# Performance work log

Hardware: AMD Instinct MI355X
Metric: run time of the kernel (lower is better)

Reference implementation:

```python
import jax, jax.numpy as jnp
import numpy as np

N_NODES = 50000
N_EDGES = 800000
D_FEAT = 128
K_HOPS = 2


def setup_inputs() -> dict:
    key = jax.random.key(0)
    k1, k2, k3 = jax.random.split(key, 3)
    features = jax.random.normal(k1, (N_NODES, D_FEAT), dtype=jnp.float32)
    src = jax.random.randint(k2, (N_EDGES,), 0, N_NODES, dtype=jnp.int64)
    dst = jax.random.randint(k3, (N_EDGES,), 0, N_NODES, dtype=jnp.int64)
    return {"features": features, "src": src, "dst": dst}


def reference(features, src, dst):
    """SGCLayer: k=2 hops, degree-normalized copy_u/sum aggregation, mean layer aggr."""
    n = features.shape[0]
    # in_degrees: number of incoming edges per node, clamped to >= 1
    deg = jax.ops.segment_sum(jnp.ones(dst.shape, dtype=features.dtype), dst,
                              num_segments=n)
    norm = jnp.power(jnp.clip(deg, 1.0), -0.5)[:, None]  # [N, 1]
    h = features
    results = [features]
    for _ in range(K_HOPS):
        h = h * norm                   # pre-scale by D^-1/2
        m = h[src]                     # copy_u: gather source features [E, F]
        h = jax.ops.segment_sum(m, dst, num_segments=n)  # sum into dst [N, F]
        h = h * norm                   # post-scale by D^-1/2
        results.append(h)
    # layer_aggr == 'mean': average over the k+1 propagated representations
    H = jnp.stack(results, axis=1)     # [N, k+1, F]
    return jnp.mean(H, axis=1)
```

## Files before the change

### kernel.cpp

```cpp
#include <hip/hip_runtime.h>

#define N_NODES 50000
#define N_EDGES 800000
#define D_FEAT  128
#define CNT_STRIDE 16
#define ELL_CAP 64

typedef unsigned int uint;
typedef unsigned short ushort_t;

union f32u { float f; uint u; };

__device__ __forceinline__ ushort_t f2bf(float f) {
    f32u x; x.f = f;
    uint u = x.u;
    return (ushort_t)((u + 0x7FFFu + ((u >> 16) & 1u)) >> 16);
}

__global__ void zero_cnt(int4* __restrict__ cnt4) {
    int i = blockIdx.x * 256 + threadIdx.x;
    if (i < N_NODES * CNT_STRIDE / 4) cnt4[i] = make_int4(0, 0, 0, 0);
}

__global__ void prep(const float4* __restrict__ feat4, const int* __restrict__ dst,
                     const int* __restrict__ src, int* __restrict__ cnt,
                     int* __restrict__ ell, ushort4* __restrict__ featb4) {
    int gid = blockIdx.x * 256 + threadIdx.x;
    bool edge = (gid < N_EDGES);
    int d = 0, p = 0;
    if (edge) {
        d = dst[gid];
        p = atomicAdd(&cnt[d * CNT_STRIDE], 1);
    }
    if (gid < N_NODES * (D_FEAT / 4)) {
        float4 v = feat4[gid];
        ushort4 o;
        o.x = f2bf(v.x); o.y = f2bf(v.y); o.z = f2bf(v.z); o.w = f2bf(v.w);
        featb4[gid] = o;
    }
    if (edge && p < ELL_CAP) ell[d * ELL_CAP + p] = src[gid];
}

__global__ void norm_scale(const int* __restrict__ cnt, float* __restrict__ norm,
                           uint4* __restrict__ featb4) {
    int j = blockIdx.x * 256 + threadIdx.x;
    if (j < N_NODES * (D_FEAT / 8)) {
        int n = j >> 4;
        int deg = cnt[n * CNT_STRIDE];
        float nn = rsqrtf((float)(deg < 1 ? 1 : deg));
        uint4 v = featb4[j];
        f32u l0, h0, l1, h1, l2, h2, l3, h3;
        l0.u = v.x << 16; h0.u = v.x & 0xFFFF0000u;
        l1.u = v.y << 16; h1.u = v.y & 0xFFFF0000u;
        l2.u = v.z << 16; h2.u = v.z & 0xFFFF0000u;
        l3.u = v.w << 16; h3.u = v.w & 0xFFFF0000u;
        uint4 o;
        o.x = (uint)f2bf(l0.f * nn) | ((uint)f2bf(h0.f * nn) << 16);
        o.y = (uint)f2bf(l1.f * nn) | ((uint)f2bf(h1.f * nn) << 16);
        o.z = (uint)f2bf(l2.f * nn) | ((uint)f2bf(h2.f * nn) << 16);
        o.w = (uint)f2bf(l3.f * nn) | ((uint)f2bf(h3.f * nn) << 16);
        featb4[j] = o;
        if (j < N_NODES) {
            int dj = cnt[j * CNT_STRIDE];
            norm[j] = rsqrtf((float)(dj < 1 ? 1 : dj));
        }
    }
}

template<int FINAL>
__global__ void hop_gather(const int* __restrict__ ell, const int* __restrict__ cnt,
                           const ushort_t* __restrict__ hb, const float* __restrict__ norm,
                           const float* __restrict__ feat, const ushort_t* __restrict__ s1,
                           void* __restrict__ outp) {
    int node = blockIdx.x * 4 + (threadIdx.x >> 6);
    int lane = threadIdx.x & 63;
    int q    = lane >> 4;
    int l16  = lane & 15;
    const uint4* hbv = (const uint4*)hb;
    int b    = node * ELL_CAP;
    int ecnt = cnt[node * CNT_STRIDE];
    if (ecnt > ELL_CAP) ecnt = ELL_CAP;
    float a0 = 0, a1 = 0, a2 = 0, a3 = 0, a4 = 0, a5 = 0, a6 = 0, a7 = 0;

#define ACC2(P, E_, O_) { f32u lo_, hi_; lo_.u = (P) << 16; hi_.u = (P) & 0xFFFF0000u; \
                          E_ += lo_.f; O_ += hi_.f; }
#define ACCV(V) { ACC2(V.x, a0, a1); ACC2(V.y, a2, a3); ACC2(V.z, a4, a5); ACC2(V.w, a6, a7); }

    int i = 0;
    for (; i + 16 <= ecnt; i += 16) {
        int s0 = ell[b + i      + q];
        int s1i = ell[b + i + 4  + q];
        int s2 = ell[b + i + 8  + q];
        int s3 = ell[b + i + 12 + q];
        uint4 v0 = hbv[s0 * 16 + l16];
        uint4 v1 = hbv[s1i * 16 + l16];
        uint4 v2 = hbv[s2 * 16 + l16];
        uint4 v3 = hbv[s3 * 16 + l16];
        ACCV(v0); ACCV(v1); ACCV(v2); ACCV(v3);
    }
    if (i + 8 <= ecnt) {
        int s0 = ell[b + i     + q];
        int s1i = ell[b + i + 4 + q];
        uint4 v0 = hbv[s0 * 16 + l16];
        uint4 v1 = hbv[s1i * 16 + l16];
        ACCV(v0); ACCV(v1);
        i += 8;
    }
    if (i + 4 <= ecnt) {
        int s_ = ell[b + i + q];
        uint4 v_ = hbv[s_ * 16 + l16];
        ACCV(v_);
        i += 4;
    }
    int rem = ecnt - i;
    if (q < rem) {
        int s_ = ell[b + i + q];
        uint4 v_ = hbv[s_ * 16 + l16];
        ACCV(v_);
    }
#undef ACCV
#undef ACC2

    a0 += __shfl_xor(a0, 16, 64); a1 += __shfl_xor(a1, 16, 64);
    a2 += __shfl_xor(a2, 16, 64); a3 += __shfl_xor(a3, 16, 64);
    a4 += __shfl_xor(a4, 16, 64); a5 += __shfl_xor(a5, 16, 64);
    a6 += __shfl_xor(a6, 16, 64); a7 += __shfl_xor(a7, 16, 64);
    a0 += __shfl_xor(a0, 32, 64); a1 += __shfl_xor(a1, 32, 64);
    a2 += __shfl_xor(a2, 32, 64); a3 += __shfl_xor(a3, 32, 64);
    a4 += __shfl_xor(a4, 32, 64); a5 += __shfl_xor(a5, 32, 64);
    a6 += __shfl_xor(a6, 32, 64); a7 += __shfl_xor(a7, 32, 64);

    if (q == 0) {
        float nn = norm[node];
        if (!FINAL) {
            float n2 = nn * nn;
            uint4 o;
            o.x = (uint)f2bf(a0 * n2) | ((uint)f2bf(a1 * n2) << 16);
            o.y = (uint)f2bf(a2 * n2) | ((uint)f2bf(a3 * n2) << 16);
            o.z = (uint)f2bf(a4 * n2) | ((uint)f2bf(a5 * n2) << 16);
            o.w = (uint)f2bf(a6 * n2) | ((uint)f2bf(a7 * n2) << 16);
            ((uint4*)outp)[node * 16 + l16] = o;
        } else {
            float inv = 1.0f / nn;
            uint4 p = ((const uint4*)s1)[node * 16 + l16];
            f32u t0, t1, t2, t3, t4, t5, t6, t7;
            t0.u = p.x << 16; t1.u = p.x & 0xFFFF0000u;
            t2.u = p.y << 16; t3.u = p.y & 0xFFFF0000u;
            t4.u = p.z << 16; t5.u = p.z & 0xFFFF0000u;
            t6.u = p.w << 16; t7.u = p.w & 0xFFFF0000u;
            const float4* f4 = (const float4*)feat;
            float4 fA = f4[node * 32 + 2 * l16];
            float4 fB = f4[node * 32 + 2 * l16 + 1];
            const float third = 1.0f / 3.0f;
            float4 rA, rB;
            rA.x = (fA.x + t0.f * inv + nn * a0) * third;
            rA.y = (fA.y + t1.f * inv + nn * a1) * third;
            rA.z = (fA.z + t2.f * inv + nn * a2) * third;
            rA.w = (fA.w + t3.f * inv + nn * a3) * third;
            rB.x = (fB.x + t4.f * inv + nn * a4) * third;
            rB.y = (fB.y + t5.f * inv + nn * a5) * third;
            rB.z = (fB.z + t6.f * inv + nn * a6) * third;
            rB.w = (fB.w + t7.f * inv + nn * a7) * third;
            ((float4*)outp)[node * 32 + 2 * l16]     = rA;
            ((float4*)outp)[node * 32 + 2 * l16 + 1] = rB;
        }
    }
}

extern "C" void kernel_launch(void* const* d_in, const int* in_sizes, int n_in,
                              void* d_out, int out_size, void* d_ws, size_t ws_size,
                              hipStream_t stream) {
    const float* feat = (const float*)d_in[0];
    const int*   src  = (const int*)d_in[1];
    const int*   dst  = (const int*)d_in[2];
    float* out = (float*)d_out;

    char* ws = (char*)d_ws;
    int*      cnt   = (int*)     (ws + 0x0000000);
    float*    norm  = (float*)   (ws + 0x0310000);
    int*      ell   = (int*)     (ws + 0x0350000);
    ushort_t* featb = (ushort_t*)(ws + 0x1000000);
    ushort_t* s1b   = (ushort_t*)(ws + 0x1D00000);

    zero_cnt<<<(N_NODES * CNT_STRIDE / 4 + 255) / 256, 256, 0, stream>>>((int4*)cnt);
    prep<<<(N_NODES * (D_FEAT / 4) + 255) / 256, 256, 0, stream>>>(
        (const float4*)feat, dst, src, cnt, ell, (ushort4*)featb);
    norm_scale<<<(N_NODES * (D_FEAT / 8) + 255) / 256, 256, 0, stream>>>(
        cnt, norm, (uint4*)featb);

    hop_gather<0><<<N_NODES / 4, 256, 0, stream>>>(ell, cnt, featb, norm,
                                                   nullptr, nullptr, s1b);
    hop_gather<1><<<N_NODES / 4, 256, 0, stream>>>(ell, cnt, s1b, norm,
                                                   feat, s1b, out);
}
```

Before: 122.2 us.

## Build ELL via two-level bucket staging with LDS histogram instead of global atomics

Replaces per-edge global atomicAdd on a padded count array with a two-pass bucketing scheme. In the first pass, wave ballots group edges by coarse destination bucket and write packed (local dst, src) pairs into aliased staging buffers. In the second pass, one 1024-thread block per bucket ranks edges with shared-memory atomics and writes the ELL table and compact counts. This removes 800K contended global atomics and the zeroing of a large padded count array. In exchange the second pass runs on only 13 blocks, which badly underuses the GPU and may serialize. Staging slots are capped at 5120, so buckets with more edges than that silently drop them. The 16-bit packing of src assumes node ids below 65536.

```diff
diff --git a/kernel.cpp b/kernel.cpp
--- a/kernel.cpp
+++ b/kernel.cpp
@@ -3,8 +3,10 @@
 #define N_NODES 50000
 #define N_EDGES 800000
 #define D_FEAT  128
-#define CNT_STRIDE 16
 #define ELL_CAP 64
+#define NBKT 13
+#define NALIAS 16
+#define STAGE_CAP 5120
 
 typedef unsigned int uint;
 typedef unsigned short ushort_t;
@@ -17,28 +19,80 @@
     return (ushort_t)((u + 0x7FFFu + ((u >> 16) & 1u)) >> 16);
 }
 
-__global__ void zero_cnt(int4* __restrict__ cnt4) {
-    int i = blockIdx.x * 256 + threadIdx.x;
-    if (i < N_NODES * CNT_STRIDE / 4) cnt4[i] = make_int4(0, 0, 0, 0);
+__global__ void zero_bcnt(int* __restrict__ bcnt) {
+    int i = threadIdx.x;
+    if (i < NBKT * NALIAS) bcnt[i] = 0;
 }
 
 __global__ void prep(const float4* __restrict__ feat4, const int* __restrict__ dst,
-                     const int* __restrict__ src, int* __restrict__ cnt,
-                     int* __restrict__ ell, ushort4* __restrict__ featb4) {
+                     const int* __restrict__ src, int* __restrict__ bcnt,
+                     uint* __restrict__ stage, ushort4* __restrict__ featb4) {
     int gid = blockIdx.x * 256 + threadIdx.x;
-    bool edge = (gid < N_EDGES);
-    int d = 0, p = 0;
-    if (edge) {
-        d = dst[gid];
-        p = atomicAdd(&cnt[d * CNT_STRIDE], 1);
-    }
+    int lane = threadIdx.x & 63;
+    bool valid = (gid < N_EDGES);
+    int d = 0;
+    if (valid) d = dst[gid];
+    int mybkt = d >> 12;
+    unsigned long long my_mask = 0;
+#pragma unroll
+    for (int b = 0; b < NBKT; b++) {
+        unsigned long long m = __ballot(valid && (mybkt == b));
+        if (mybkt == b) my_mask = m;
+    }
+    int leader = __ffsll(my_mask) - 1;
+    if (leader < 0) leader = 0;
+    int grpcnt = __popcll(my_mask);
+    int alias = blockIdx.x & (NALIAS - 1);
+    int base_reg = 0;
+    if (valid && lane == leader)
+        base_reg = atomicAdd(&bcnt[mybkt * NALIAS + alias], grpcnt);
+
     if (gid < N_NODES * (D_FEAT / 4)) {
         float4 v = feat4[gid];
         ushort4 o;
         o.x = f2bf(v.x); o.y = f2bf(v.y); o.z = f2bf(v.z); o.w = f2bf(v.w);
         featb4[gid] = o;
     }
-    if (edge && p < ELL_CAP) ell[d * ELL_CAP + p] = src[gid];
+
+    int base = __shfl(base_reg, leader, 64);
+    int rank = __popcll(my_mask & ((1ull << lane) - 1));
+    if (valid) {
+        int slot = base + rank;
+        if (slot < STAGE_CAP) {
+            int s = src[gid];
+            stage[(mybkt * NALIAS + alias) * STAGE_CAP + slot] =
+                ((uint)(d & 4095) << 16) | (uint)s;
+        }
+    }
+}
+
+__global__ __launch_bounds__(1024) void bucket_rank(const int* __restrict__ bcnt,
+                                                    const uint* __restrict__ stage,
+                                                    int* __restrict__ ell,
+                                                    int* __restrict__ cnt) {
+    __shared__ int hist[4096];
+    int b = blockIdx.x;
+    for (int i = threadIdx.x; i < 4096; i += 1024) hist[i] = 0;
+    __syncthreads();
+    for (int a = 0; a < NALIAS; a++) {
+        int n = bcnt[b * NALIAS + a];
+        if (n > STAGE_CAP) n = STAGE_CAP;
+        const uint* sp = stage + (b * NALIAS + a) * STAGE_CAP;
+        for (int i = threadIdx.x; i < n; i += 1024) {
+            uint v = sp[i];
+            int ldst = v >> 16;
+            int s = (int)(v & 0xFFFFu);
+            int p = atomicAdd(&hist[ldst], 1);
+            if (p < ELL_CAP)
+                ell[(((b << 12) + ldst) << 6) + p] = s;
+        }
+    }
+    __syncthreads();
+    int base_node = b << 12;
+    for (int i = threadIdx.x; i < 4096; i += 1024) {
+        int n = base_node + i;
+        if (n < N_NODES) cnt[n] = hist[i];
+    }
 }
 
 __global__ void norm_scale(const int* __restrict__ cnt, float* __restrict__ norm,
@@ -46,7 +100,7 @@
     int j = blockIdx.x * 256 + threadIdx.x;
     if (j < N_NODES * (D_FEAT / 8)) {
         int n = j >> 4;
-        int deg = cnt[n * CNT_STRIDE];
+        int deg = cnt[n];
         float nn = rsqrtf((float)(deg < 1 ? 1 : deg));
         uint4 v = featb4[j];
         f32u l0, h0, l1, h1, l2, h2, l3, h3;
@@ -61,7 +115,7 @@
         o.w = (uint)f2bf(l3.f * nn) | ((uint)f2bf(h3.f * nn) << 16);
         featb4[j] = o;
         if (j < N_NODES) {
-            int dj = cnt[j * CNT_STRIDE];
+            int dj = cnt[j];
             norm[j] = rsqrtf((float)(dj < 1 ? 1 : dj));
         }
     }
@@ -78,7 +132,7 @@
     int l16  = lane & 15;
     const uint4* hbv = (const uint4*)hb;
     int b    = node * ELL_CAP;
-    int ecnt = cnt[node * CNT_STRIDE];
+    int ecnt = cnt[node];
     if (ecnt > ELL_CAP) ecnt = ELL_CAP;
     float a0 = 0, a1 = 0, a2 = 0, a3 = 0, a4 = 0, a5 = 0, a6 = 0, a7 = 0;
 
@@ -176,15 +230,18 @@
     float* out = (float*)d_out;
 
     char* ws = (char*)d_ws;
-    int*      cnt   = (int*)     (ws + 0x0000000);
-    float*    norm  = (float*)   (ws + 0x0310000);
-    int*      ell   = (int*)     (ws + 0x0350000);
-    ushort_t* featb = (ushort_t*)(ws + 0x1000000);
-    ushort_t* s1b   = (ushort_t*)(ws + 0x1D00000);
-
-    zero_cnt<<<(N_NODES * CNT_STRIDE / 4 + 255) / 256, 256, 0, stream>>>((int4*)cnt);
+    int*      bcnt  = (int*)     (ws + 0x0000000);
+    int*      cnt   = (int*)     (ws + 0x0010000);
+    float*    norm  = (float*)   (ws + 0x0050000);
+    uint*     stage = (uint*)    (ws + 0x0090000);
+    int*      ell   = (int*)     (ws + 0x0500000);
+    ushort_t* featb = (ushort_t*)(ws + 0x1200000);
+    ushort_t* s1b   = (ushort_t*)(ws + 0x1F00000);
+
+    zero_bcnt<<<1, 256, 0, stream>>>(bcnt);
     prep<<<(N_NODES * (D_FEAT / 4) + 255) / 256, 256, 0, stream>>>(
-        (const float4*)feat, dst, src, cnt, ell, (ushort4*)featb);
+        (const float4*)feat, dst, src, bcnt, stage, (ushort4*)featb);
+    bucket_rank<<<NBKT, 1024, 0, stream>>>(bcnt, stage, ell, cnt);
     norm_scale<<<(N_NODES * (D_FEAT / 8) + 255) / 256, 256, 0, stream>>>(
         cnt, norm, (uint4*)featb);
 
```

Result: slower. 380.3 us (+211.2%).

## Build ELL adjacency via per-block LDS histograms over destination ranges

Applied to the files above, without the earlier changes.

Replaces the global-atomic ELL build, which needed a zeroing kernel and a strided count array, with 64 blocks that each scan all edges and use shared-memory atomics for their own 784-node destination range. Degree counts and norms are written directly, and the bf16 conversion is fused with the norm pre-scale into a single kernel. This removes two launches and the contention from global atomics. In exchange every block re-reads the full src/dst arrays (64x redundant reads), and only 64 blocks run, so parallelism across the GPU is low.

```diff
diff --git a/kernel.cpp b/kernel.cpp
--- a/kernel.cpp
+++ b/kernel.cpp
@@ -3,8 +3,9 @@
 #define N_NODES 50000
 #define N_EDGES 800000
 #define D_FEAT  128
-#define CNT_STRIDE 16
 #define ELL_CAP 64
+#define NB 64
+#define RANGE 784
 
 typedef unsigned int uint;
 typedef unsigned short ushort_t;
@@ -17,53 +18,48 @@
     return (ushort_t)((u + 0x7FFFu + ((u >> 16) & 1u)) >> 16);
 }
 
-__global__ void zero_cnt(int4* __restrict__ cnt4) {
-    int i = blockIdx.x * 256 + threadIdx.x;
-    if (i < N_NODES * CNT_STRIDE / 4) cnt4[i] = make_int4(0, 0, 0, 0);
+__global__ __launch_bounds__(256) void ell_build(const int4* __restrict__ src4,
+                                                 const int4* __restrict__ dst4,
+                                                 int* __restrict__ ell,
+                                                 int* __restrict__ cnt,
+                                                 float* __restrict__ norm) {
+    __shared__ int hist[RANGE];
+    int lo = blockIdx.x * RANGE;
+    for (int i = threadIdx.x; i < RANGE; i += 256) hist[i] = 0;
+    __syncthreads();
+    for (int i = threadIdx.x; i < N_EDGES / 4; i += 256) {
+        int4 d4 = dst4[i];
+        int4 s4 = src4[i];
+#define DO(c) { int d_ = d4.c; unsigned r_ = (unsigned)(d_ - lo);              \
+                if (r_ < RANGE) {                                              \
+                    int p_ = atomicAdd(&hist[r_], 1);                          \
+                    if (p_ < ELL_CAP) ell[d_ * ELL_CAP + p_] = s4.c;           \
+                } }
+        DO(x) DO(y) DO(z) DO(w)
+#undef DO
+    }
+    __syncthreads();
+    for (int i = threadIdx.x; i < RANGE; i += 256) {
+        int n = lo + i;
+        if (n < N_NODES) {
+            int c = hist[i];
+            cnt[n] = c;
+            norm[n] = rsqrtf((float)(c < 1 ? 1 : c));
+        }
+    }
 }
 
-__global__ void prep(const float4* __restrict__ feat4, const int* __restrict__ dst,
-                     const int* __restrict__ src, int* __restrict__ cnt,
-                     int* __restrict__ ell, ushort4* __restrict__ featb4) {
+__global__ void convert_scale(const float4* __restrict__ feat4,
+                              const float* __restrict__ norm,
+                              ushort4* __restrict__ featb4) {
     int gid = blockIdx.x * 256 + threadIdx.x;
-    bool edge = (gid < N_EDGES);
-    int d = 0, p = 0;
-    if (edge) {
-        d = dst[gid];
-        p = atomicAdd(&cnt[d * CNT_STRIDE], 1);
-    }
     if (gid < N_NODES * (D_FEAT / 4)) {
+        float nn = norm[gid >> 5];
         float4 v = feat4[gid];
         ushort4 o;
-        o.x = f2bf(v.x); o.y = f2bf(v.y); o.z = f2bf(v.z); o.w = f2bf(v.w);
+        o.x = f2bf(v.x * nn); o.y = f2bf(v.y * nn);
+        o.z = f2bf(v.z * nn); o.w = f2bf(v.w * nn);
         featb4[gid] = o;
-    }
-    if (edge && p < ELL_CAP) ell[d * ELL_CAP + p] = src[gid];
-}
-
-__global__ void norm_scale(const int* __restrict__ cnt, float* __restrict__ norm,
-                           uint4* __restrict__ featb4) {
-    int j = blockIdx.x * 256 + threadIdx.x;
-    if (j < N_NODES * (D_FEAT / 8)) {
-        int n = j >> 4;
-        int deg = cnt[n * CNT_STRIDE];
-        float nn = rsqrtf((float)(deg < 1 ? 1 : deg));
-        uint4 v = featb4[j];
-        f32u l0, h0, l1, h1, l2, h2, l3, h3;
-        l0.u = v.x << 16; h0.u = v.x & 0xFFFF0000u;
-        l1.u = v.y << 16; h1.u = v.y & 0xFFFF0000u;
-        l2.u = v.z << 16; h2.u = v.z & 0xFFFF0000u;
-        l3.u = v.w << 16; h3.u = v.w & 0xFFFF0000u;
-        uint4 o;
-        o.x = (uint)f2bf(l0.f * nn) | ((uint)f2bf(h0.f * nn) << 16);
-        o.y = (uint)f2bf(l1.f * nn) | ((uint)f2bf(h1.f * nn) << 16);
-        o.z = (uint)f2bf(l2.f * nn) | ((uint)f2bf(h2.f * nn) << 16);
-        o.w = (uint)f2bf(l3.f * nn) | ((uint)f2bf(h3.f * nn) << 16);
-        featb4[j] = o;
-        if (j < N_NODES) {
-            int dj = cnt[j * CNT_STRIDE];
-            norm[j] = rsqrtf((float)(dj < 1 ? 1 : dj));
-        }
     }
 }
 
@@ -78,7 +74,7 @@
     int l16  = lane & 15;
     const uint4* hbv = (const uint4*)hb;
     int b    = node * ELL_CAP;
-    int ecnt = cnt[node * CNT_STRIDE];
+    int ecnt = cnt[node];
     if (ecnt > ELL_CAP) ecnt = ELL_CAP;
     float a0 = 0, a1 = 0, a2 = 0, a3 = 0, a4 = 0, a5 = 0, a6 = 0, a7 = 0;
 
@@ -177,16 +173,15 @@
 
     char* ws = (char*)d_ws;
     int*      cnt   = (int*)     (ws + 0x0000000);
-    float*    norm  = (float*)   (ws + 0x0310000);
-    int*      ell   = (int*)     (ws + 0x0350000);
-    ushort_t* featb = (ushort_t*)(ws + 0x1000000);
-    ushort_t* s1b   = (ushort_t*)(ws + 0x1D00000);
+    float*    norm  = (float*)   (ws + 0x0040000);
+    int*      ell   = (int*)     (ws + 0x0080000);
+    ushort_t* featb = (ushort_t*)(ws + 0x0D80000);
+    ushort_t* s1b   = (ushort_t*)(ws + 0x1A80000);
 
-    zero_cnt<<<(N_NODES * CNT_STRIDE / 4 + 255) / 256, 256, 0, stream>>>((int4*)cnt);
-    prep<<<(N_NODES * (D_FEAT / 4) + 255) / 256, 256, 0, stream>>>(
-        (const float4*)feat, dst, src, cnt, ell, (ushort4*)featb);
-    norm_scale<<<(N_NODES * (D_FEAT / 8) + 255) / 256, 256, 0, stream>>>(
-        cnt, norm, (uint4*)featb);
+    ell_build<<<NB, 256, 0, stream>>>((const int4*)src, (const int4*)dst,
+                                      ell, cnt, norm);
+    convert_scale<<<(N_NODES * (D_FEAT / 4) + 255) / 256, 256, 0, stream>>>(
+        (const float4*)feat, norm, (ushort4*)featb);
 
     hop_gather<0><<<N_NODES / 4, 256, 0, stream>>>(ell, cnt, featb, norm,
                                                    nullptr, nullptr, s1b);
```

New measurement: 448.8 us. 3.67x slower.
